# Performance work log

Hardware: AMD Instinct MI355X
Metric: run time of the kernel (lower is better)

Reference implementation:

```python
import jax, jax.numpy as jnp
import numpy as np

T, D, E, K = 8192, 4096, 64, 8


def setup_inputs() -> dict:
    key = jax.random.key(0)
    k1, k2, k3, k4 = jax.random.split(key, 4)
    x = jax.random.normal(k1, (T, D), dtype=jnp.float32)
    # nn.Linear stores weight as [out_features, in_features]
    Wg = jax.random.normal(k2, (E, D), dtype=jnp.float32) * (1.0 / np.sqrt(D))
    Wc = jax.random.normal(k3, (E, D), dtype=jnp.float32) * (1.0 / np.sqrt(D))
    extra_scale = jnp.zeros((E,), dtype=jnp.float32)  # init zeros as in module
    extra_bias = jax.random.normal(k4, (E,), dtype=jnp.float32) * 0.01
    return {"x": x, "Wg": Wg, "Wc": Wc, "extra_scale": extra_scale,
            "extra_bias": extra_bias, "topk": K}


def reference(x, Wg, Wc, extra_scale, extra_bias, topk):
    # scores = |classifier(x) * silu(gate(x))|, softmax in fp32
    gate = jnp.einsum('td,ed->te', x, Wg)        # [T, E]
    cls = jnp.einsum('td,ed->te', x, Wc)         # [T, E]
    scores = jnp.abs(cls * jax.nn.silu(gate))
    scores = jax.nn.softmax(scores.astype(jnp.float32), axis=-1)
    biased = scores + extra_bias[None, :]        # load-balance bias, used only for selection
    _, indices = jax.lax.top_k(biased, topk)     # [T, K]
    original = 1.0 + scores * extra_scale[None, :]
    weights = jnp.take_along_axis(original, indices, axis=1)  # [T, K]
    return weights.astype(x.dtype), indices
```

## Files before the change

### kernel.cpp

```cpp
#include <hip/hip_runtime.h>
#include <math.h>


#define T_DIM 8192
#define D_DIM 4096
#define E_DIM 64
#define N2    128
#define MB    128
#define BK    32
#define LDA   140
#define KTOP  8

__device__ __forceinline__ int SW(int m) { return m + ((m >> 5) << 2); }

template<int KS>
__global__ __launch_bounds__(256, 2)
void router_gemm(const float* __restrict__ x,
                 const float* __restrict__ Wg,
                 const float* __restrict__ Wc,
                 float* __restrict__ P)
{
    constexpr int SLICEK = D_DIM / KS;
    constexpr int NS     = SLICEK / BK;

    __shared__ float sx[BK][LDA];
    __shared__ float sw[BK][LDA];

    const int tid = threadIdx.x;
    const int mb  = blockIdx.x;
    const int ks  = blockIdx.y;

    const int r2 = tid >> 1;
    const int kq = tid & 1;

    const int k0 = ks * SLICEK;

    const float4* xp = (const float4*)(x + (size_t)(mb * MB + r2) * D_DIM + k0 + kq * 16);
    const float*  wrow = (r2 < E_DIM) ? (Wg + (size_t)r2 * D_DIM)
                                      : (Wc + (size_t)(r2 - E_DIM) * D_DIM);
    const float4* wp = (const float4*)(wrow + k0 + kq * 16);

    float4 rx[4], rw[4];
    #pragma unroll
    for (int q = 0; q < 4; ++q) { rx[q] = xp[q]; rw[q] = wp[q]; }

    float acc[8][8];
    #pragma unroll
    for (int i = 0; i < 8; ++i)
        #pragma unroll
        for (int j = 0; j < 8; ++j) acc[i][j] = 0.f;

    const int tm8 = (tid & 15) * 8;
    const int tn8 = (tid >> 4) * 8;
    const int smx = SW(tm8);
    const int snx = SW(tn8);
    const int swr = SW(r2);

    for (int s = 0; s < NS; ++s) {
        #pragma unroll
        for (int q = 0; q < 4; ++q) {
            const int k = kq * 16 + q * 4;
            sx[k+0][swr] = rx[q].x; sx[k+1][swr] = rx[q].y;
            sx[k+2][swr] = rx[q].z; sx[k+3][swr] = rx[q].w;
            sw[k+0][swr] = rw[q].x; sw[k+1][swr] = rw[q].y;
            sw[k+2][swr] = rw[q].z; sw[k+3][swr] = rw[q].w;
        }
        __syncthreads();

        if (s + 1 < NS) {
            xp += 8; wp += 8;
            #pragma unroll
            for (int q = 0; q < 4; ++q) { rx[q] = xp[q]; rw[q] = wp[q]; }
        }

        #pragma unroll
        for (int kk = 0; kk < BK; ++kk) {
            const float4 a0 = *(const float4*)&sx[kk][smx];
            const float4 a1 = *(const float4*)&sx[kk][smx + 4];
            const float4 b0 = *(const float4*)&sw[kk][snx];
            const float4 b1 = *(const float4*)&sw[kk][snx + 4];
            const float a[8] = {a0.x,a0.y,a0.z,a0.w,a1.x,a1.y,a1.z,a1.w};
            const float b[8] = {b0.x,b0.y,b0.z,b0.w,b1.x,b1.y,b1.z,b1.w};
            #pragma unroll
            for (int i = 0; i < 8; ++i)
                #pragma unroll
                for (int j = 0; j < 8; ++j)
                    acc[i][j] = fmaf(a[i], b[j], acc[i][j]);
        }
        __syncthreads();
    }

    float* Pr = P + ((size_t)ks * T_DIM + (size_t)mb * MB + tm8) * N2 + tn8;
    #pragma unroll
    for (int i = 0; i < 8; ++i) {
        const float4 s0 = make_float4(acc[i][0], acc[i][1], acc[i][2], acc[i][3]);
        const float4 s1 = make_float4(acc[i][4], acc[i][5], acc[i][6], acc[i][7]);
        *(float4*)&Pr[(size_t)i * N2]     = s0;
        *(float4*)&Pr[(size_t)i * N2 + 4] = s1;
    }
}

template<int KS>
__global__ __launch_bounds__(256)
void router_topk(const float* __restrict__ P,
                 const float* __restrict__ scale,
                 const float* __restrict__ bias,
                 float* __restrict__ out)
{
    const int lane = threadIdx.x & 63;
    const int wid  = threadIdx.x >> 6;
    const int row  = blockIdx.x * 4 + wid;

    float gv[KS], cv[KS];
    #pragma unroll
    for (int ks = 0; ks < KS; ++ks) {
        const float* p = P + ((size_t)ks * T_DIM + row) * N2;
        gv[ks] = p[lane];
        cv[ks] = p[E_DIM + lane];
    }
    float g = 0.f, c = 0.f;
    #pragma unroll
    for (int ks = 0; ks < KS; ++ks) { g += gv[ks]; c += cv[ks]; }

    const float sg = g / (1.f + expf(-g));
    const float v  = fabsf(c * sg);

    float m = v;
    #pragma unroll
    for (int off = 32; off >= 1; off >>= 1) m = fmaxf(m, __shfl_xor(m, off));
    const float e = expf(v - m);
    float Z = e;
    #pragma unroll
    for (int off = 32; off >= 1; off >>= 1) Z += __shfl_xor(Z, off);
    const float s = e / Z;

    const float sc  = scale[lane];
    float cur = s + bias[lane];

    float myw = 0.f; int myi = 0;
    #pragma unroll
    for (int j = 0; j < KTOP; ++j) {
        float bv = cur; int bi = lane;
        #pragma unroll
        for (int off = 32; off >= 1; off >>= 1) {
            const float ov = __shfl_xor(bv, off);
            const int   oi = __shfl_xor(bi, off);
            if (ov > bv || (ov == bv && oi < bi)) { bv = ov; bi = oi; }
        }
        const float s_bi  = __shfl(s,  bi);
        const float sc_bi = __shfl(sc, bi);
        const float w = 1.f + s_bi * sc_bi;
        if (lane == j)  { myw = w; myi = bi; }
        if (lane == bi) cur = -INFINITY;
    }

    if (lane < KTOP) {
        out[(size_t)row * KTOP + lane] = myw;
        out[(size_t)T_DIM * KTOP + (size_t)row * KTOP + lane] = (float)myi;
    }
}

template<int KS>
static void launch_all(const float* x, const float* Wg, const float* Wc,
                       const float* sc, const float* bs,
                       float* out, float* P, hipStream_t stream)
{
    dim3 g1(T_DIM / MB, KS);
    router_gemm<KS><<<g1, 256, 0, stream>>>(x, Wg, Wc, P);
    router_topk<KS><<<T_DIM / 4, 256, 0, stream>>>(P, sc, bs, out);
}

extern "C" void kernel_launch(void* const* d_in, const int* in_sizes, int n_in,
                              void* d_out, int out_size, void* d_ws, size_t ws_size,
                              hipStream_t stream)
{
    const float* x  = (const float*)d_in[0];
    const float* Wg = (const float*)d_in[1];
    const float* Wc = (const float*)d_in[2];
    const float* sc = (const float*)d_in[3];
    const float* bs = (const float*)d_in[4];
    float* out = (float*)d_out;
    float* P   = (float*)d_ws;

    const size_t per = (size_t)T_DIM * N2 * sizeof(float);
    int ksplit = 16;
    while (ksplit > 1 && (size_t)ksplit * per > ws_size) ksplit >>= 1;

    switch (ksplit) {
        case 16: launch_all<16>(x, Wg, Wc, sc, bs, out, P, stream); break;
        case 8:  launch_all<8>(x, Wg, Wc, sc, bs, out, P, stream); break;
        case 4:  launch_all<4>(x, Wg, Wc, sc, bs, out, P, stream); break;
        case 2:  launch_all<2>(x, Wg, Wc, sc, bs, out, P, stream); break;
        default: launch_all<1>(x, Wg, Wc, sc, bs, out, P, stream); break;
    }
}
```

Before: 282.8 us.

## Use split-bf16 MFMA GEMM with exact fp32 fallback for near-tie rows

Replaces the fp32 FMA SIMT GEMM with a 3-way bf16 split (six MFMA products) on matrix cores, reading x directly from global memory without LDS staging. Weights are pre-split into hi/mid/lo bf16 planes by a new kernel, and the split-K factor drops from 16 to 8. In the top-k kernel, rows whose selection gap is below a threshold are recomputed with an exact fp32 dot product to keep index choices consistent. This trades some precision and an extra pass plus an occasional slow fallback for much higher matrix throughput.

```diff
diff --git a/kernel.cpp b/kernel.cpp
--- a/kernel.cpp
+++ b/kernel.cpp
@@ -7,97 +7,133 @@
 #define E_DIM 64
 #define N2    128
 #define MB    128
-#define BK    32
-#define LDA   140
 #define KTOP  8
-
-__device__ __forceinline__ int SW(int m) { return m + ((m >> 5) << 2); }
+#define GAP_THRESH 2e-6f
+
+typedef __bf16 bf16x8 __attribute__((ext_vector_type(8)));
+typedef __bf16 bf16x4 __attribute__((ext_vector_type(4)));
+typedef float  f32x4  __attribute__((ext_vector_type(4)));
+
+__global__ __launch_bounds__(256)
+void wsplit(const float* __restrict__ Wg, const float* __restrict__ Wc,
+            __bf16* __restrict__ WH, __bf16* __restrict__ WM,
+            __bf16* __restrict__ WL)
+{
+    const size_t i    = ((size_t)blockIdx.x * 256 + threadIdx.x) * 4;
+    const size_t half = (size_t)E_DIM * D_DIM;
+    const float4 v = (i < half) ? ((const float4*)Wg)[i >> 2]
+                                : ((const float4*)Wc)[(i - half) >> 2];
+    const float f[4] = {v.x, v.y, v.z, v.w};
+    bf16x4 hv, mv, lv;
+    #pragma unroll
+    for (int j = 0; j < 4; ++j) {
+        const __bf16 h = (__bf16)f[j];
+        const float r1 = f[j] - (float)h;
+        const __bf16 m = (__bf16)r1;
+        const float r2 = r1 - (float)m;
+        hv[j] = h; mv[j] = m; lv[j] = (__bf16)r2;
+    }
+    *(bf16x4*)(WH + i) = hv;
+    *(bf16x4*)(WM + i) = mv;
+    *(bf16x4*)(WL + i) = lv;
+}
+
+__device__ __forceinline__ void split3_8(const float4 a, const float4 b,
+                                         bf16x8& h, bf16x8& m, bf16x8& l)
+{
+    const float f[8] = {a.x, a.y, a.z, a.w, b.x, b.y, b.z, b.w};
+    #pragma unroll
+    for (int j = 0; j < 8; ++j) {
+        const __bf16 hj = (__bf16)f[j];
+        const float r1 = f[j] - (float)hj;
+        const __bf16 mj = (__bf16)r1;
+        const float r2 = r1 - (float)mj;
+        h[j] = hj; m[j] = mj; l[j] = (__bf16)r2;
+    }
+}
 
 template<int KS>
-__global__ __launch_bounds__(256, 2)
+__global__ __launch_bounds__(256)
 void router_gemm(const float* __restrict__ x,
-                 const float* __restrict__ Wg,
-                 const float* __restrict__ Wc,
+                 const __bf16* __restrict__ WH,
+                 const __bf16* __restrict__ WM,
+                 const __bf16* __restrict__ WL,
                  float* __restrict__ P)
 {
     constexpr int SLICEK = D_DIM / KS;
-    constexpr int NS     = SLICEK / BK;
-
-    __shared__ float sx[BK][LDA];
-    __shared__ float sw[BK][LDA];
-
-    const int tid = threadIdx.x;
-    const int mb  = blockIdx.x;
-    const int ks  = blockIdx.y;
-
-    const int r2 = tid >> 1;
-    const int kq = tid & 1;
-
-    const int k0 = ks * SLICEK;
-
-    const float4* xp = (const float4*)(x + (size_t)(mb * MB + r2) * D_DIM + k0 + kq * 16);
-    const float*  wrow = (r2 < E_DIM) ? (Wg + (size_t)r2 * D_DIM)
-                                      : (Wc + (size_t)(r2 - E_DIM) * D_DIM);
-    const float4* wp = (const float4*)(wrow + k0 + kq * 16);
-
-    float4 rx[4], rw[4];
-    #pragma unroll
-    for (int q = 0; q < 4; ++q) { rx[q] = xp[q]; rw[q] = wp[q]; }
-
-    float acc[8][8];
-    #pragma unroll
-    for (int i = 0; i < 8; ++i)
-        #pragma unroll
-        for (int j = 0; j < 8; ++j) acc[i][j] = 0.f;
-
-    const int tm8 = (tid & 15) * 8;
-    const int tn8 = (tid >> 4) * 8;
-    const int smx = SW(tm8);
-    const int snx = SW(tn8);
-    const int swr = SW(r2);
-
-    for (int s = 0; s < NS; ++s) {
-        #pragma unroll
-        for (int q = 0; q < 4; ++q) {
-            const int k = kq * 16 + q * 4;
-            sx[k+0][swr] = rx[q].x; sx[k+1][swr] = rx[q].y;
-            sx[k+2][swr] = rx[q].z; sx[k+3][swr] = rx[q].w;
-            sw[k+0][swr] = rw[q].x; sw[k+1][swr] = rw[q].y;
-            sw[k+2][swr] = rw[q].z; sw[k+3][swr] = rw[q].w;
-        }
-        __syncthreads();
-
-        if (s + 1 < NS) {
-            xp += 8; wp += 8;
+    constexpr int NSTEP  = SLICEK / 32;
+
+    const int lane = threadIdx.x & 63;
+    const int wid  = threadIdx.x >> 6;
+    const int mb   = blockIdx.x;
+    const int ks   = blockIdx.y;
+
+    const int m0   = mb * MB + wid * 32;
+    const int mrow = lane & 15;
+    const int quad = lane >> 4;
+    const int k0   = ks * SLICEK + quad * 8;
+
+    const float* xa0 = x + (size_t)(m0 +      mrow) * D_DIM + k0;
+    const float* xa1 = x + (size_t)(m0 + 16 + mrow) * D_DIM + k0;
+    const size_t bofs = (size_t)mrow * D_DIM + k0;
+
+    f32x4 acc[2][8];
+    #pragma unroll
+    for (int mt = 0; mt < 2; ++mt)
+        #pragma unroll
+        for (int nt = 0; nt < 8; ++nt)
+            acc[mt][nt] = (f32x4){0.f, 0.f, 0.f, 0.f};
+
+    float4 p00 = *(const float4*)(xa0);
+    float4 p01 = *(const float4*)(xa0 + 4);
+    float4 p10 = *(const float4*)(xa1);
+    float4 p11 = *(const float4*)(xa1 + 4);
+
+    for (int s = 0; s < NSTEP; ++s) {
+        bf16x8 a0h, a0m, a0l, a1h, a1m, a1l;
+        split3_8(p00, p01, a0h, a0m, a0l);
+        split3_8(p10, p11, a1h, a1m, a1l);
+
+        if (s + 1 < NSTEP) {
+            const int kn = (s + 1) * 32;
+            p00 = *(const float4*)(xa0 + kn);
+            p01 = *(const float4*)(xa0 + kn + 4);
+            p10 = *(const float4*)(xa1 + kn);
+            p11 = *(const float4*)(xa1 + kn + 4);
+        }
+
+        const int kk = s * 32;
+        #pragma unroll
+        for (int nt = 0; nt < 8; ++nt) {
+            const size_t bo = bofs + (size_t)nt * 16 * D_DIM + kk;
+            const bf16x8 BH = *(const bf16x8*)(WH + bo);
+            const bf16x8 BM = *(const bf16x8*)(WM + bo);
+            const bf16x8 BL = *(const bf16x8*)(WL + bo);
+            acc[0][nt] = __builtin_amdgcn_mfma_f32_16x16x32_bf16(a0h, BH, acc[0][nt], 0, 0, 0);
+            acc[0][nt] = __builtin_amdgcn_mfma_f32_16x16x32_bf16(a0h, BM, acc[0][nt], 0, 0, 0);
+            acc[0][nt] = __builtin_amdgcn_mfma_f32_16x16x32_bf16(a0m, BH, acc[0][nt], 0, 0, 0);
+            acc[0][nt] = __builtin_amdgcn_mfma_f32_16x16x32_bf16(a0h, BL, acc[0][nt], 0, 0, 0);
+            acc[0][nt] = __builtin_amdgcn_mfma_f32_16x16x32_bf16(a0m, BM, acc[0][nt], 0, 0, 0);
+            acc[0][nt] = __builtin_amdgcn_mfma_f32_16x16x32_bf16(a0l, BH, acc[0][nt], 0, 0, 0);
+            acc[1][nt] = __builtin_amdgcn_mfma_f32_16x16x32_bf16(a1h, BH, acc[1][nt], 0, 0, 0);
+            acc[1][nt] = __builtin_amdgcn_mfma_f32_16x16x32_bf16(a1h, BM, acc[1][nt], 0, 0, 0);
+            acc[1][nt] = __builtin_amdgcn_mfma_f32_16x16x32_bf16(a1m, BH, acc[1][nt], 0, 0, 0);
+            acc[1][nt] = __builtin_amdgcn_mfma_f32_16x16x32_bf16(a1h, BL, acc[1][nt], 0, 0, 0);
+            acc[1][nt] = __builtin_amdgcn_mfma_f32_16x16x32_bf16(a1m, BM, acc[1][nt], 0, 0, 0);
+            acc[1][nt] = __builtin_amdgcn_mfma_f32_16x16x32_bf16(a1l, BH, acc[1][nt], 0, 0, 0);
+        }
+    }
+
+    #pragma unroll
+    for (int mt = 0; mt < 2; ++mt)
+        #pragma unroll
+        for (int nt = 0; nt < 8; ++nt) {
+            float* Pp = P + ((size_t)ks * T_DIM + m0 + mt * 16 + quad * 4) * N2
+                          + nt * 16 + mrow;
             #pragma unroll
-            for (int q = 0; q < 4; ++q) { rx[q] = xp[q]; rw[q] = wp[q]; }
-        }
-
-        #pragma unroll
-        for (int kk = 0; kk < BK; ++kk) {
-            const float4 a0 = *(const float4*)&sx[kk][smx];
-            const float4 a1 = *(const float4*)&sx[kk][smx + 4];
-            const float4 b0 = *(const float4*)&sw[kk][snx];
-            const float4 b1 = *(const float4*)&sw[kk][snx + 4];
-            const float a[8] = {a0.x,a0.y,a0.z,a0.w,a1.x,a1.y,a1.z,a1.w};
-            const float b[8] = {b0.x,b0.y,b0.z,b0.w,b1.x,b1.y,b1.z,b1.w};
-            #pragma unroll
-            for (int i = 0; i < 8; ++i)
-                #pragma unroll
-                for (int j = 0; j < 8; ++j)
-                    acc[i][j] = fmaf(a[i], b[j], acc[i][j]);
-        }
-        __syncthreads();
-    }
-
-    float* Pr = P + ((size_t)ks * T_DIM + (size_t)mb * MB + tm8) * N2 + tn8;
-    #pragma unroll
-    for (int i = 0; i < 8; ++i) {
-        const float4 s0 = make_float4(acc[i][0], acc[i][1], acc[i][2], acc[i][3]);
-        const float4 s1 = make_float4(acc[i][4], acc[i][5], acc[i][6], acc[i][7]);
-        *(float4*)&Pr[(size_t)i * N2]     = s0;
-        *(float4*)&Pr[(size_t)i * N2 + 4] = s1;
-    }
+            for (int r = 0; r < 4; ++r)
+                Pp[(size_t)r * N2] = acc[mt][nt][r];
+        }
 }
 
 template<int KS>
@@ -105,6 +141,9 @@
 void router_topk(const float* __restrict__ P,
                  const float* __restrict__ scale,
                  const float* __restrict__ bias,
+                 const float* __restrict__ x,
+                 const float* __restrict__ Wg,
+                 const float* __restrict__ Wc,
                  float* __restrict__ out)
 {
     const int lane = threadIdx.x & 63;
@@ -122,24 +161,25 @@
     #pragma unroll
     for (int ks = 0; ks < KS; ++ks) { g += gv[ks]; c += cv[ks]; }
 
-    const float sg = g / (1.f + expf(-g));
-    const float v  = fabsf(c * sg);
-
+    const float sc  = scale[lane];
+    const float bsv = bias[lane];
+
+    float sg = g / (1.f + expf(-g));
+    float v  = fabsf(c * sg);
     float m = v;
     #pragma unroll
     for (int off = 32; off >= 1; off >>= 1) m = fmaxf(m, __shfl_xor(m, off));
-    const float e = expf(v - m);
+    float e = expf(v - m);
     float Z = e;
     #pragma unroll
     for (int off = 32; off >= 1; off >>= 1) Z += __shfl_xor(Z, off);
-    const float s = e / Z;
-
-    const float sc  = scale[lane];
-    float cur = s + bias[lane];
+    float s = e / Z;
+    float cur = s + bsv;
 
     float myw = 0.f; int myi = 0;
-    #pragma unroll
-    for (int j = 0; j < KTOP; ++j) {
+    float prev = 0.f, mingap = 1e30f;
+    #pragma unroll
+    for (int j = 0; j < KTOP + 1; ++j) {
         float bv = cur; int bi = lane;
         #pragma unroll
         for (int off = 32; off >= 1; off >>= 1) {
@@ -147,11 +187,60 @@
             const int   oi = __shfl_xor(bi, off);
             if (ov > bv || (ov == bv && oi < bi)) { bv = ov; bi = oi; }
         }
-        const float s_bi  = __shfl(s,  bi);
-        const float sc_bi = __shfl(sc, bi);
-        const float w = 1.f + s_bi * sc_bi;
-        if (lane == j)  { myw = w; myi = bi; }
-        if (lane == bi) cur = -INFINITY;
+        if (j > 0) mingap = fminf(mingap, prev - bv);
+        prev = bv;
+        if (j < KTOP) {
+            const float s_bi  = __shfl(s,  bi);
+            const float sc_bi = __shfl(sc, bi);
+            if (lane == j)  { myw = 1.f + s_bi * sc_bi; myi = bi; }
+            if (lane == bi) cur = -INFINITY;
+        }
+    }
+
+    if (mingap < GAP_THRESH) {
+        const float* xr = x  + (size_t)row  * D_DIM;
+        const float* wg = Wg + (size_t)lane * D_DIM;
+        const float* wc = Wc + (size_t)lane * D_DIM;
+        float g0 = 0.f, g1 = 0.f, c0 = 0.f, c1 = 0.f;
+        #pragma unroll 4
+        for (int k = 0; k < D_DIM; k += 8) {
+            const float4 xv0 = *(const float4*)(xr + k);
+            const float4 xv1 = *(const float4*)(xr + k + 4);
+            const float4 wg0 = *(const float4*)(wg + k);
+            const float4 wg1 = *(const float4*)(wg + k + 4);
+            const float4 wc0 = *(const float4*)(wc + k);
+            const float4 wc1 = *(const float4*)(wc + k + 4);
+            g0 = fmaf(xv0.x, wg0.x, fmaf(xv0.y, wg0.y, fmaf(xv0.z, wg0.z, fmaf(xv0.w, wg0.w, g0))));
+            g1 = fmaf(xv1.x, wg1.x, fmaf(xv1.y, wg1.y, fmaf(xv1.z, wg1.z, fmaf(xv1.w, wg1.w, g1))));
+            c0 = fmaf(xv0.x, wc0.x, fmaf(xv0.y, wc0.y, fmaf(xv0.z, wc0.z, fmaf(xv0.w, wc0.w, c0))));
+            c1 = fmaf(xv1.x, wc1.x, fmaf(xv1.y, wc1.y, fmaf(xv1.z, wc1.z, fmaf(xv1.w, wc1.w, c1))));
+        }
+        const float ge = g0 + g1, ce = c0 + c1;
+        sg = ge / (1.f + expf(-ge));
+        v  = fabsf(ce * sg);
+        m = v;
+        #pragma unroll
+        for (int off = 32; off >= 1; off >>= 1) m = fmaxf(m, __shfl_xor(m, off));
+        e = expf(v - m);
+        Z = e;
+        #pragma unroll
+        for (int off = 32; off >= 1; off >>= 1) Z += __shfl_xor(Z, off);
+        s = e / Z;
+        cur = s + bsv;
+        #pragma unroll
+        for (int j = 0; j < KTOP; ++j) {
+            float bv = cur; int bi = lane;
+            #pragma unroll
+            for (int off = 32; off >= 1; off >>= 1) {
+                const float ov = __shfl_xor(bv, off);
+                const int   oi = __shfl_xor(bi, off);
+                if (ov > bv || (ov == bv && oi < bi)) { bv = ov; bi = oi; }
+            }
+            const float s_bi  = __shfl(s,  bi);
+            const float sc_bi = __shfl(sc, bi);
+            if (lane == j)  { myw = 1.f + s_bi * sc_bi; myi = bi; }
+            if (lane == bi) cur = -INFINITY;
+        }
     }
 
     if (lane < KTOP) {
@@ -163,11 +252,16 @@
 template<int KS>
 static void launch_all(const float* x, const float* Wg, const float* Wc,
                        const float* sc, const float* bs,
-                       float* out, float* P, hipStream_t stream)
-{
-    dim3 g1(T_DIM / MB, KS);
-    router_gemm<KS><<<g1, 256, 0, stream>>>(x, Wg, Wc, P);
-    router_topk<KS><<<T_DIM / 4, 256, 0, stream>>>(P, sc, bs, out);
+                       float* out, void* ws, hipStream_t stream)
+{
+    __bf16* WH = (__bf16*)ws;
+    __bf16* WM = WH + (size_t)N2 * D_DIM;
+    __bf16* WL = WM + (size_t)N2 * D_DIM;
+    float*  P  = (float*)(WL + (size_t)N2 * D_DIM);
+
+    wsplit<<<(N2 * D_DIM) / (256 * 4), 256, 0, stream>>>(Wg, Wc, WH, WM, WL);
+    router_gemm<KS><<<dim3(T_DIM / MB, KS), 256, 0, stream>>>(x, WH, WM, WL, P);
+    router_topk<KS><<<T_DIM / 4, 256, 0, stream>>>(P, sc, bs, x, Wg, Wc, out);
 }
 
 extern "C" void kernel_launch(void* const* d_in, const int* in_sizes, int n_in,
@@ -180,17 +274,16 @@
     const float* sc = (const float*)d_in[3];
     const float* bs = (const float*)d_in[4];
     float* out = (float*)d_out;
-    float* P   = (float*)d_ws;
-
-    const size_t per = (size_t)T_DIM * N2 * sizeof(float);
-    int ksplit = 16;
-    while (ksplit > 1 && (size_t)ksplit * per > ws_size) ksplit >>= 1;
+
+    const size_t wfix = (size_t)3 * N2 * D_DIM * sizeof(__bf16);
+    const size_t per  = (size_t)T_DIM * N2 * sizeof(float);
+    int ksplit = 8;
+    while (ksplit > 1 && wfix + (size_t)ksplit * per > ws_size) ksplit >>= 1;
 
     switch (ksplit) {
-        case 16: launch_all<16>(x, Wg, Wc, sc, bs, out, P, stream); break;
-        case 8:  launch_all<8>(x, Wg, Wc, sc, bs, out, P, stream); break;
-        case 4:  launch_all<4>(x, Wg, Wc, sc, bs, out, P, stream); break;
-        case 2:  launch_all<2>(x, Wg, Wc, sc, bs, out, P, stream); break;
-        default: launch_all<1>(x, Wg, Wc, sc, bs, out, P, stream); break;
-    }
-}
+        case 8:  launch_all<8>(x, Wg, Wc, sc, bs, out, d_ws, stream); break;
+        case 4:  launch_all<4>(x, Wg, Wc, sc, bs, out, d_ws, stream); break;
+        case 2:  launch_all<2>(x, Wg, Wc, sc, bs, out, d_ws, stream); break;
+        default: launch_all<1>(x, Wg, Wc, sc, bs, out, d_ws, stream); break;
+    }
+}
```

New measurement: 422.9 us. +49.5%, slower.
